# Optimization experiments

Hardware: AMD Instinct MI355X
Metric: run time of the kernel (lower is better)

The kernel has to match this reference:

```python
import jax, jax.numpy as jnp
import numpy as np

N = 100000       # nodes
E = 1600000      # edges
NFEAT = 128
NHID = 128
NCLASS = 64
NHEAD = 4
NLAYER = 3
LRELU_ALPHA = 0.2


def setup_inputs() -> dict:
    key = jax.random.key(0)
    ks = jax.random.split(key, 7)
    x = jax.random.normal(ks[0], (N, NFEAT), jnp.float32)
    edge_index = jax.random.randint(ks[1], (2, E), 0, N, jnp.int32)
    # xavier-uniform-ish init scales (gain for relu baked into scale roughly)
    Win = jax.random.normal(ks[2], (NFEAT, NHID), jnp.float32) * (2.0 / (NFEAT + NHID)) ** 0.5
    b_in = jnp.zeros((NHID,), jnp.float32)
    # per hidden layer, per head: a split into (src, dst) halves of the (1, 2*in) vector
    a_hid = jax.random.normal(ks[3], (NLAYER - 1, NHEAD, 2, NHID), jnp.float32) * 0.1
    W_hid = jax.random.normal(ks[4], (NLAYER - 1, NHEAD, NHID, NHID // NHEAD), jnp.float32) * (2.0 / (NHID + NHID // NHEAD)) ** 0.5
    a_out = jax.random.normal(ks[5], (2, NHID), jnp.float32) * 0.1
    W_out = jax.random.normal(ks[6], (NHID, NCLASS), jnp.float32) * (2.0 / (NHID + NCLASS)) ** 0.5
    return dict(x=x, edge_index=edge_index, Win=Win, b_in=b_in,
                a_hid=a_hid, W_hid=W_hid, a_out=a_out, W_out=W_out)


def _segment_softmax(logits, seg, n):
    # numerically stable softmax over groups defined by seg (axis 0)
    m = jax.ops.segment_max(logits, seg, num_segments=n)
    e = jnp.exp(logits - m[seg])
    s = jax.ops.segment_sum(e, seg, num_segments=n)
    return e / s[seg]


def _gat_conv(h, row, col, a, W):
    # h: [N, D]; a: [H, 2, D]; W: [H, D, Dh]
    n = h.shape[0]
    H = a.shape[0]
    s_src = h @ a[:, 0, :].T  # [N, H]
    s_dst = h @ a[:, 1, :].T  # [N, H]
    logits = jax.nn.leaky_relu(s_src[row] + s_dst[col], LRELU_ALPHA)  # [E, H]
    alpha = _segment_softmax(logits, row, n)  # softmax grouped by row (edge_index[0])
    h_col = h[col]  # [E, D] gathered once, reused per head
    outs = []
    for hd in range(H):  # small fixed head loop keeps peak memory at [E, D]
        agg = jax.ops.segment_sum(alpha[:, hd, None] * h_col, row, num_segments=n)  # [N, D]
        outs.append(agg @ W[hd])  # weight applied AFTER aggregation, as in source
    return jnp.concatenate(outs, axis=1)


def reference(x, edge_index, Win, b_in, a_hid, W_hid, a_out, W_out):
    row, col = edge_index[0], edge_index[1]
    h = jax.nn.elu(x @ Win + b_in)  # in_linear + ELU (dropout is identity in eval/p=0)
    for l in range(a_hid.shape[0]):
        h = jax.nn.elu(_gat_conv(h, row, col, a_hid[l], W_hid[l]))
    # final conv: single head to nclass, no activation
    return _gat_conv(h, row, col, a_out[None], W_out[None])
```

## Files before the change

kernel.cpp:

```cpp
#include <hip/hip_runtime.h>
#include <hip/hip_bf16.h>
#include <cstdint>
#include <cstddef>

#define LRELU_ALPHA 0.2f

typedef __attribute__((ext_vector_type(8))) short short8;
typedef __attribute__((ext_vector_type(4))) float f32x4;

__device__ __forceinline__ unsigned short f2bf(float f) {
    unsigned int u = __float_as_uint(f);
    unsigned int r = (u + 0x7fffu + ((u >> 16) & 1u)) >> 16;
    return (unsigned short)r;
}
__device__ __forceinline__ float bf2f(unsigned int lo16) {
    return __uint_as_float(lo16 << 16);
}
__device__ __forceinline__ unsigned int pk2(float a, float b) {
    return (unsigned int)f2bf(a) | ((unsigned int)f2bf(b) << 16);
}


__global__ void hist_k(const int* __restrict__ ei, int* __restrict__ counts,
                       int* __restrict__ rank, int E_) {
    int e = blockIdx.x * 256 + threadIdx.x;
    if (e < E_) {
        int r = ei[e];
        rank[e] = atomicAdd(&counts[r], 1);
    }
}

__global__ void scan_block_k(const int* __restrict__ counts, int* __restrict__ tmp,
                             int* __restrict__ bsum, int n) {
    __shared__ int s[256];
    int i = blockIdx.x * 256 + threadIdx.x;
    int v = (i < n) ? counts[i] : 0;
    s[threadIdx.x] = v;
    __syncthreads();
    for (int d = 1; d < 256; d <<= 1) {
        int t_ = (threadIdx.x >= d) ? s[threadIdx.x - d] : 0;
        __syncthreads();
        s[threadIdx.x] += t_;
        __syncthreads();
    }
    if (i < n) tmp[i] = s[threadIdx.x];
    if (threadIdx.x == 255) bsum[blockIdx.x] = s[255];
}

__global__ void scan_sums_k(int* bsum, int nb) {
    __shared__ int s[512];
    int v = ((int)threadIdx.x < nb) ? bsum[threadIdx.x] : 0;
    s[threadIdx.x] = v;
    __syncthreads();
    for (int d = 1; d < 512; d <<= 1) {
        int t_ = ((int)threadIdx.x >= d) ? s[threadIdx.x - d] : 0;
        __syncthreads();
        s[threadIdx.x] += t_;
        __syncthreads();
    }
    if ((int)threadIdx.x < nb) bsum[threadIdx.x] = s[threadIdx.x] - v;
}

__global__ void finalize_k(const int* __restrict__ tmp, const int* __restrict__ bsum,
                           int* __restrict__ off, int n) {
    int i = blockIdx.x * 256 + threadIdx.x;
    if (i < n) off[i + 1] = tmp[i] + bsum[blockIdx.x];
    if (i == 0) off[0] = 0;
}

__global__ void scatter_k(const int* __restrict__ ei, const int* __restrict__ rank,
                          const int* __restrict__ off, int* __restrict__ scol, int E_) {
    int e = blockIdx.x * 256 + threadIdx.x;
    if (e < E_) {
        int r = ei[e];
        int pos = off[r] + rank[e];
        scol[pos] = ei[E_ + e];
    }
}


template <int KJ, int HD>
__global__ void repack_wt(const float* __restrict__ src, unsigned short* __restrict__ wt) {
    int i = blockIdx.x * 256 + threadIdx.x;
    if (i < KJ * 128) {
        int n = i >> 7, k = i & 127;
        constexpr int JW = KJ / HD;
        int hd = n / JW, j = n % JW;
        wt[i] = f2bf(src[(hd * 128 + k) * JW + j]);
    }
}


template <int KJ, bool ELU_ACT, bool BIAS, bool BF16_OUT, bool ABF16>
__global__ __launch_bounds__(256) void gemm_mfma(const void* __restrict__ Xv,
                                                 const unsigned short* __restrict__ WT,
                                                 const float* __restrict__ bias,
                                                 void* __restrict__ Yv, int nRows) {
    constexpr int NT = KJ / 16;
    constexpr int WS = 136;
    __shared__ unsigned short sWT[KJ * WS];
    int t = threadIdx.x;
    for (int i = t; i < KJ * 16; i += 256) {
        int n = i >> 4, k8 = i & 15;
        uint4 v = *(const uint4*)&WT[n * 128 + k8 * 8];
        *(uint4*)&sWT[n * WS + k8 * 8] = v;
    }
    __syncthreads();

    int lane = t & 63;
    int wv = t >> 6;
    int m0 = blockIdx.x * 128 + wv * 32;
    int l16 = lane & 15;
    int q4 = lane >> 4;

    short8 afr[4][2];
    #pragma unroll
    for (int rt = 0; rt < 2; rt++) {
        int row = m0 + rt * 16 + l16;
        bool vr = row < nRows;
        if (ABF16) {
            const unsigned int* xp = (const unsigned int*)Xv + (size_t)row * 64 + q4 * 4;
            #pragma unroll
            for (int kk = 0; kk < 4; kk++) {
                uint4 u = make_uint4(0u, 0u, 0u, 0u);
                if (vr) u = *(const uint4*)(xp + kk * 16);
                afr[kk][rt] = *(short8*)&u;
            }
        } else {
            const float* xp = (const float*)Xv + (size_t)row * 128 + q4 * 8;
            #pragma unroll
            for (int kk = 0; kk < 4; kk++) {
                float4 a0 = make_float4(0.f, 0.f, 0.f, 0.f), a1 = a0;
                if (vr) {
                    a0 = *(const float4*)(xp + kk * 32);
                    a1 = *(const float4*)(xp + kk * 32 + 4);
                }
                unsigned int u[4];
                u[0] = pk2(a0.x, a0.y); u[1] = pk2(a0.z, a0.w);
                u[2] = pk2(a1.x, a1.y); u[3] = pk2(a1.z, a1.w);
                afr[kk][rt] = *(short8*)u;
            }
        }
    }

    f32x4 acc[2][NT] = {};
    #pragma unroll
    for (int kk = 0; kk < 4; kk++) {
        #pragma unroll
        for (int ct = 0; ct < NT; ct++) {
            int n = ct * 16 + l16;
            short8 bf = *(const short8*)&sWT[n * WS + kk * 32 + q4 * 8];
            #pragma unroll
            for (int rt = 0; rt < 2; rt++)
                acc[rt][ct] = __builtin_amdgcn_mfma_f32_16x16x32_bf16(afr[kk][rt], bf, acc[rt][ct], 0, 0, 0);
        }
    }

    #pragma unroll
    for (int rt = 0; rt < 2; rt++) {
        #pragma unroll
        for (int q = 0; q < 4; q++) {
            int row = m0 + rt * 16 + q4 * 4 + q;
            if (row >= nRows) continue;
            #pragma unroll
            for (int ct = 0; ct < NT; ct++) {
                int colc = ct * 16 + l16;
                float v = acc[rt][ct][q];
                if (BIAS) v += bias[colc];
                if (ELU_ACT) v = v > 0.f ? v : (__expf(v) - 1.f);
                if (BF16_OUT) ((unsigned short*)Yv)[(size_t)row * KJ + colc] = f2bf(v);
                else          ((float*)Yv)[(size_t)row * KJ + colc] = v;
            }
        }
    }
}


template <int H>
__global__ __launch_bounds__(256) void attn_scores_bf(const unsigned int* __restrict__ h2,
                                                      const float* __restrict__ a,
                                                      float* __restrict__ s_src,
                                                      float* __restrict__ s_dst, int n) {
    __shared__ float sa[H * 2 * 128];
    for (int i = threadIdx.x; i < H * 2 * 128; i += 256) sa[i] = a[i];
    __syncthreads();
    int lane = threadIdx.x & 63, wv = threadIdx.x >> 6;
    int node = blockIdx.x * 4 + wv;
    if (node >= n) return;
    unsigned int hv = h2[(size_t)node * 64 + lane];
    float v0 = bf2f(hv & 0xffffu), v1 = bf2f(hv >> 16);
    #pragma unroll
    for (int hd = 0; hd < H; hd++) {
        #pragma unroll
        for (int side = 0; side < 2; side++) {
            const float2 aa = *(const float2*)&sa[(hd * 2 + side) * 128 + 2 * lane];
            float p = v0 * aa.x + v1 * aa.y;
            #pragma unroll
            for (int s = 32; s > 0; s >>= 1) p += __shfl_xor(p, s);
            if (lane == 0) {
                float* dst = side ? s_dst : s_src;
                dst[node * H + hd] = p;
            }
        }
    }
}


template <int DHT, int H, bool ELU_ACT, int HN, bool BF16O>
__global__ __launch_bounds__(256) void edge_agg_v(const unsigned int* __restrict__ hW2,
                                                  const float* __restrict__ ssrc,
                                                  const float* __restrict__ sdst,
                                                  const int* __restrict__ off,
                                                  const int* __restrict__ scol,
                                                  void* __restrict__ outv,
                                                  const float* __restrict__ a_next,
                                                  float* __restrict__ ssrc_n,
                                                  float* __restrict__ sdst_n, int nRows) {
    constexpr int FPL = DHT / 16;
    constexpr int UPL = FPL / 2;
    constexpr int NC = (HN > 0) ? 2 * HN : 1;
    __shared__ float sAN[NC * 128];
    if (HN > 0) {
        for (int i = threadIdx.x; i < NC * 128; i += 256) sAN[i] = a_next[i];
        __syncthreads();
    }
    int lane = threadIdx.x & 63;
    int sub = lane & 15;
    int g = lane >> 4;
    int wv = threadIdx.x >> 6;
    int r = __builtin_amdgcn_readfirstlane(blockIdx.x * 4 + wv);
    if (r >= nRows) return;
    int begin = off[r], end = off[r + 1];

    int head = (H == 4) ? (sub >> 2) : 0;
    float ssl = ssrc[r * H + head];

    float acc[FPL] = {};
    float den = 0.f;

    for (int i = begin; i < end; i += 8) {
        int iA = i + g, iB = i + 4 + g;
        bool vA = iA < end, vB = iB < end;
        int cA = scol[vA ? iA : begin];
        int cB = scol[vB ? iB : begin];
        float sdA = sdst[cA * H + head];
        float sdB = sdst[cB * H + head];
        unsigned int hA[UPL], hB[UPL];
        int oA = cA * (DHT / 2) + sub * UPL;
        int oB = cB * (DHT / 2) + sub * UPL;
        if (UPL == 4) {
            *(uint4*)hA = *(const uint4*)&hW2[oA];
            *(uint4*)hB = *(const uint4*)&hW2[oB];
        } else {
            *(uint2*)hA = *(const uint2*)&hW2[oA];
            *(uint2*)hB = *(const uint2*)&hW2[oB];
        }
        float lgA = ssl + sdA; lgA = lgA > 0.f ? lgA : LRELU_ALPHA * lgA;
        float wA = vA ? __expf(lgA) : 0.f;
        float lgB = ssl + sdB; lgB = lgB > 0.f ? lgB : LRELU_ALPHA * lgB;
        float wB = vB ? __expf(lgB) : 0.f;
        den += wA + wB;
        #pragma unroll
        for (int q = 0; q < UPL; q++) {
            acc[2 * q]     = fmaf(wA, bf2f(hA[q] & 0xffffu), acc[2 * q]);
            acc[2 * q + 1] = fmaf(wA, bf2f(hA[q] >> 16),     acc[2 * q + 1]);
            acc[2 * q]     = fmaf(wB, bf2f(hB[q] & 0xffffu), acc[2 * q]);
            acc[2 * q + 1] = fmaf(wB, bf2f(hB[q] >> 16),     acc[2 * q + 1]);
        }
    }

    #pragma unroll
    for (int s = 16; s < 64; s <<= 1) {
        den += __shfl_xor(den, s);
        #pragma unroll
        for (int p = 0; p < FPL; p++) acc[p] += __shfl_xor(acc[p], s);
    }
    float inv = den > 0.f ? 1.f / den : 0.f;

    float v[FPL];
    #pragma unroll
    for (int p = 0; p < FPL; p++) {
        float tv = acc[p] * inv;
        if (ELU_ACT) tv = tv > 0.f ? tv : (__expf(tv) - 1.f);
        v[p] = tv;
    }

    if (DHT == 128) {
        if (BF16O)
            ((unsigned int*)outv)[(size_t)r * 64 + sub * 4 + g] = pk2(v[2 * g], v[2 * g + 1]);
        else
            *(float2*)&((float*)outv)[(size_t)r * 128 + sub * 8 + 2 * g] =
                make_float2(v[2 * g], v[2 * g + 1]);
    } else {
        ((float*)outv)[(size_t)r * DHT + sub * FPL + g] = v[g];
    }

    if (HN > 0) {
        constexpr int CPG = (HN == 4) ? 2 : 1;
        #pragma unroll
        for (int cc = 0; cc < CPG; cc++) {
            int c = (HN == 4) ? (g * 2 + cc) : (g & 1);
            const float* ap = &sAN[c * 128 + sub * FPL];
            float partial = 0.f;
            #pragma unroll
            for (int p = 0; p < FPL; p++) partial += v[p] * ap[p];
            #pragma unroll
            for (int s = 1; s < 16; s <<= 1) partial += __shfl_xor(partial, s);
            if (sub == 0 && (HN == 4 || g < 2)) {
                int hd = c >> 1;
                float* dst = (c & 1) ? sdst_n : ssrc_n;
                dst[r * HN + hd] = partial;
            }
        }
    }
}


extern "C" void kernel_launch(void* const* d_in, const int* in_sizes, int n_in,
                              void* d_out, int out_size, void* d_ws, size_t ws_size,
                              hipStream_t stream) {
    const float* x    = (const float*)d_in[0];
    const int*   ei   = (const int*)d_in[1];
    const float* Win  = (const float*)d_in[2];
    const float* bin  = (const float*)d_in[3];
    const float* ahid = (const float*)d_in[4];
    const float* Whid = (const float*)d_in[5];
    const float* aout = (const float*)d_in[6];
    const float* Wout = (const float*)d_in[7];
    float* out = (float*)d_out;

    const int N_ = in_sizes[0] / 128;
    const int E_ = in_sizes[1] / 2;

    char* p = (char*)d_ws;
    auto alloc = [&](size_t bytes) {
        char* q = p;
        p += (bytes + 511) & ~(size_t)511;
        return q;
    };
    int* counts = (int*)alloc((size_t)N_ * 4);
    int* tmp    = (int*)alloc((size_t)N_ * 4);
    int* rank   = (int*)alloc((size_t)E_ * 4);
    int* off    = (int*)alloc((size_t)(N_ + 1) * 4);
    int* bsum   = (int*)alloc(4096);
    int* scol   = (int*)alloc((size_t)(E_ + 8) * 4);
    float* ssrcA = (float*)alloc((size_t)N_ * 4 * 4);
    float* sdstA = (float*)alloc((size_t)N_ * 4 * 4);
    float* ssrcB = (float*)alloc((size_t)N_ * 4 * 4);
    float* sdstB = (float*)alloc((size_t)N_ * 4 * 4);
    unsigned int* hb  = (unsigned int*)alloc((size_t)N_ * 64 * 4);
    unsigned int* hWb = (unsigned int*)alloc((size_t)N_ * 64 * 4);
    unsigned short* WTb = (unsigned short*)alloc(128 * 128 * 2);

    int NB = (N_ + 255) / 256;
    int EB = (E_ + 255) / 256;
    int RT = (N_ + 127) / 128;
    int NW = (N_ + 3) / 4;

    hipMemsetAsync(counts, 0, (size_t)N_ * 4, stream);
    hist_k<<<EB, 256, 0, stream>>>(ei, counts, rank, E_);
    scan_block_k<<<NB, 256, 0, stream>>>(counts, tmp, bsum, N_);
    scan_sums_k<<<1, 512, 0, stream>>>(bsum, NB);
    finalize_k<<<NB, 256, 0, stream>>>(tmp, bsum, off, N_);
    scatter_k<<<EB, 256, 0, stream>>>(ei, rank, off, scol, E_);

    repack_wt<128, 1><<<64, 256, 0, stream>>>(Win, WTb);
    gemm_mfma<128, true, true, true, false><<<RT, 256, 0, stream>>>(x, WTb, bin, hb, N_);

    attn_scores_bf<4><<<NW, 256, 0, stream>>>(hb, ahid, ssrcA, sdstA, N_);

    repack_wt<128, 4><<<64, 256, 0, stream>>>(Whid, WTb);
    gemm_mfma<128, false, false, true, true><<<RT, 256, 0, stream>>>(hb, WTb, nullptr, hWb, N_);
    edge_agg_v<128, 4, true, 4, true><<<NW, 256, 0, stream>>>(
        hWb, ssrcA, sdstA, off, scol, hb, ahid + 4 * 2 * 128, ssrcB, sdstB, N_);

    repack_wt<128, 4><<<64, 256, 0, stream>>>(Whid + (size_t)4 * 128 * 32, WTb);
    gemm_mfma<128, false, false, true, true><<<RT, 256, 0, stream>>>(hb, WTb, nullptr, hWb, N_);
    edge_agg_v<128, 4, true, 1, true><<<NW, 256, 0, stream>>>(
        hWb, ssrcB, sdstB, off, scol, hb, aout, ssrcA, sdstA, N_);

    repack_wt<64, 1><<<32, 256, 0, stream>>>(Wout, WTb);
    gemm_mfma<64, false, false, true, true><<<RT, 256, 0, stream>>>(hb, WTb, nullptr, hWb, N_);
    edge_agg_v<64, 1, false, 0, false><<<NW, 256, 0, stream>>>(
        hWb, ssrcA, sdstA, off, scol, out, nullptr, nullptr, nullptr, N_);
}
```

Baseline: 522.4 us.

## Pad CSR rows to multiples of 8, use fp16 dot2 aggregation and exp2 scores

```diff
diff --git a/kernel.cpp b/kernel.cpp
--- a/kernel.cpp
+++ b/kernel.cpp
@@ -4,9 +4,11 @@
 #include <cstddef>
 
 #define LRELU_ALPHA 0.2f
+#define LOG2E 1.44269504088896f
 
 typedef __attribute__((ext_vector_type(8))) short short8;
 typedef __attribute__((ext_vector_type(4))) float f32x4;
+typedef _Float16 h2v __attribute__((ext_vector_type(2)));
 
 __device__ __forceinline__ unsigned short f2bf(float f) {
     unsigned int u = __float_as_uint(f);
@@ -18,6 +20,46 @@
 }
 __device__ __forceinline__ unsigned int pk2(float a, float b) {
     return (unsigned int)f2bf(a) | ((unsigned int)f2bf(b) << 16);
+}
+__device__ __forceinline__ float fexp2(float x) {
+#if __has_builtin(__builtin_amdgcn_exp2f)
+    return __builtin_amdgcn_exp2f(x);
+#else
+    return __expf(x * 0.69314718056f);
+#endif
+}
+__device__ __forceinline__ h2v pkrtz(float a, float b) {
+#if __has_builtin(__builtin_amdgcn_cvt_pkrtz)
+    auto r = __builtin_amdgcn_cvt_pkrtz(a, b);
+    union { decltype(r) i; h2v o; } u;
+    u.i = r;
+    return u.o;
+#else
+    h2v r; r.x = (_Float16)a; r.y = (_Float16)b; return r;
+#endif
+}
+__device__ __forceinline__ unsigned int pack_lo(unsigned int a, unsigned int b) {
+#if __has_builtin(__builtin_amdgcn_perm)
+    return __builtin_amdgcn_perm(a, b, 0x01000504u);
+#else
+    return (a & 0xffffu) | (b << 16);
+#endif
+}
+__device__ __forceinline__ unsigned int pack_hi(unsigned int a, unsigned int b) {
+#if __has_builtin(__builtin_amdgcn_perm)
+    return __builtin_amdgcn_perm(a, b, 0x03020706u);
+#else
+    return (a >> 16) | (b & 0xffff0000u);
+#endif
+}
+union U32H2 { unsigned int u; h2v h; };
+__device__ __forceinline__ float dot2f(unsigned int a, h2v w, float acc) {
+    U32H2 c; c.u = a;
+#if __has_builtin(__builtin_amdgcn_fdot2)
+    return __builtin_amdgcn_fdot2(c.h, w, acc, false);
+#else
+    return acc + (float)c.h.x * (float)w.x + (float)c.h.y * (float)w.y;
+#endif
 }
 
 
@@ -30,11 +72,25 @@
     }
 }
 
+__global__ void fill_pad_k(int* __restrict__ scol, float* __restrict__ sdA,
+                           float* __restrict__ sdB, float* __restrict__ sdC,
+                           unsigned int* __restrict__ hW, int N_, int total) {
+    int i = blockIdx.x * 256 + threadIdx.x;
+    if (i < total) scol[i] = N_;
+    if (blockIdx.x == 0) {
+        int t = threadIdx.x;
+        if (t < 4) { sdA[N_ * 4 + t] = -1e30f; sdB[N_ * 4 + t] = -1e30f; }
+        if (t == 4) sdC[N_] = -1e30f;
+        if (t >= 32 && t < 64)  hW[(size_t)N_ * 32 + (t - 32)] = 0u;
+        if (t >= 64 && t < 128) hW[(size_t)N_ * 64 + (t - 64)] = 0u;
+    }
+}
+
 __global__ void scan_block_k(const int* __restrict__ counts, int* __restrict__ tmp,
                              int* __restrict__ bsum, int n) {
     __shared__ int s[256];
     int i = blockIdx.x * 256 + threadIdx.x;
-    int v = (i < n) ? counts[i] : 0;
+    int v = (i < n) ? ((counts[i] + 7) & ~7) : 0;
     s[threadIdx.x] = v;
     __syncthreads();
     for (int d = 1; d < 256; d <<= 1) {
@@ -79,19 +135,31 @@
 }
 
 
-template <int KJ, int HD>
-__global__ void repack_wt(const float* __restrict__ src, unsigned short* __restrict__ wt) {
+__global__ void repack_all(const float* __restrict__ Win, const float* __restrict__ Whid,
+                           const float* __restrict__ Wout,
+                           unsigned short* __restrict__ W0, unsigned short* __restrict__ W1,
+                           unsigned short* __restrict__ W2, unsigned short* __restrict__ W3) {
     int i = blockIdx.x * 256 + threadIdx.x;
-    if (i < KJ * 128) {
+    if (i < 16384) {
         int n = i >> 7, k = i & 127;
-        constexpr int JW = KJ / HD;
-        int hd = n / JW, j = n % JW;
-        wt[i] = f2bf(src[(hd * 128 + k) * JW + j]);
-    }
-}
-
-
-template <int KJ, bool ELU_ACT, bool BIAS, bool BF16_OUT, bool ABF16>
+        W0[i] = f2bf(Win[k * 128 + n]);
+    } else if (i < 49152) {
+        int j = i - 16384;
+        int l = j >> 14;
+        int jj = j & 16383;
+        int n = jj >> 7, k = jj & 127;
+        int hd = n >> 5, c = n & 31;
+        float v = Whid[(size_t)l * 16384 + (hd * 128 + k) * 32 + c];
+        (l ? W2 : W1)[jj] = f2bf(v);
+    } else if (i < 57344) {
+        int j = i - 49152;
+        int n = j >> 7, k = j & 127;
+        W3[j] = f2bf(Wout[k * 64 + n]);
+    }
+}
+
+
+template <int KJ, bool ELU_ACT, bool BIAS, int OUTM, bool ABF16>
 __global__ __launch_bounds__(256) void gemm_mfma(const void* __restrict__ Xv,
                                                  const unsigned short* __restrict__ WT,
                                                  const float* __restrict__ bias,
@@ -168,8 +236,15 @@
                 float v = acc[rt][ct][q];
                 if (BIAS) v += bias[colc];
                 if (ELU_ACT) v = v > 0.f ? v : (__expf(v) - 1.f);
-                if (BF16_OUT) ((unsigned short*)Yv)[(size_t)row * KJ + colc] = f2bf(v);
-                else          ((float*)Yv)[(size_t)row * KJ + colc] = v;
+                if (OUTM == 1) {
+                    ((unsigned short*)Yv)[(size_t)row * KJ + colc] = f2bf(v);
+                } else if (OUTM == 2) {
+                    union { _Float16 hf; unsigned short us; } cv;
+                    cv.hf = (_Float16)v;
+                    ((unsigned short*)Yv)[(size_t)row * KJ + colc] = cv.us;
+                } else {
+                    ((float*)Yv)[(size_t)row * KJ + colc] = v;
+                }
             }
         }
     }
@@ -177,30 +252,35 @@
 
 
 template <int H>
-__global__ __launch_bounds__(256) void attn_scores_bf(const unsigned int* __restrict__ h2,
-                                                      const float* __restrict__ a,
-                                                      float* __restrict__ s_src,
-                                                      float* __restrict__ s_dst, int n) {
+__global__ __launch_bounds__(256) void attn_scores16(const unsigned int* __restrict__ h2,
+                                                     const float* __restrict__ a,
+                                                     float* __restrict__ s_src,
+                                                     float* __restrict__ s_dst, int n) {
     __shared__ float sa[H * 2 * 128];
-    for (int i = threadIdx.x; i < H * 2 * 128; i += 256) sa[i] = a[i];
+    for (int i = threadIdx.x; i < H * 2 * 128; i += 256) sa[i] = a[i] * LOG2E;
     __syncthreads();
     int lane = threadIdx.x & 63, wv = threadIdx.x >> 6;
-    int node = blockIdx.x * 4 + wv;
-    if (node >= n) return;
-    unsigned int hv = h2[(size_t)node * 64 + lane];
-    float v0 = bf2f(hv & 0xffffu), v1 = bf2f(hv >> 16);
-    #pragma unroll
-    for (int hd = 0; hd < H; hd++) {
-        #pragma unroll
-        for (int side = 0; side < 2; side++) {
-            const float2 aa = *(const float2*)&sa[(hd * 2 + side) * 128 + 2 * lane];
-            float p = v0 * aa.x + v1 * aa.y;
-            #pragma unroll
-            for (int s = 32; s > 0; s >>= 1) p += __shfl_xor(p, s);
-            if (lane == 0) {
-                float* dst = side ? s_dst : s_src;
-                dst[node * H + hd] = p;
-            }
+    int sub = lane & 15, g = lane >> 4;
+    int node = (blockIdx.x * 4 + wv) * 4 + g;
+    bool valid = node < n;
+    int nd = valid ? node : 0;
+    uint4 hv = *(const uint4*)&h2[(size_t)nd * 64 + sub * 4];
+    float f[8];
+    f[0] = bf2f(hv.x & 0xffffu); f[1] = bf2f(hv.x >> 16);
+    f[2] = bf2f(hv.y & 0xffffu); f[3] = bf2f(hv.y >> 16);
+    f[4] = bf2f(hv.z & 0xffffu); f[5] = bf2f(hv.z >> 16);
+    f[6] = bf2f(hv.w & 0xffffu); f[7] = bf2f(hv.w >> 16);
+    #pragma unroll
+    for (int c = 0; c < 2 * H; c++) {
+        const float* ap = &sa[c * 128 + sub * 8];
+        float p = 0.f;
+        #pragma unroll
+        for (int q = 0; q < 8; q++) p += f[q] * ap[q];
+        #pragma unroll
+        for (int s = 1; s < 16; s <<= 1) p += __shfl_xor(p, s);
+        if (sub == 0 && valid) {
+            float* dst = (c & 1) ? s_dst : s_src;
+            dst[node * H + (c >> 1)] = p;
         }
     }
 }
@@ -221,7 +301,7 @@
     constexpr int NC = (HN > 0) ? 2 * HN : 1;
     __shared__ float sAN[NC * 128];
     if (HN > 0) {
-        for (int i = threadIdx.x; i < NC * 128; i += 256) sAN[i] = a_next[i];
+        for (int i = threadIdx.x; i < NC * 128; i += 256) sAN[i] = a_next[i] * LOG2E;
         __syncthreads();
     }
     int lane = threadIdx.x & 63;
@@ -239,10 +319,8 @@
     float den = 0.f;
 
     for (int i = begin; i < end; i += 8) {
-        int iA = i + g, iB = i + 4 + g;
-        bool vA = iA < end, vB = iB < end;
-        int cA = scol[vA ? iA : begin];
-        int cB = scol[vB ? iB : begin];
+        int2 cc = *(const int2*)&scol[i + 2 * g];
+        int cA = cc.x, cB = cc.y;
         float sdA = sdst[cA * H + head];
         float sdB = sdst[cB * H + head];
         unsigned int hA[UPL], hB[UPL];
@@ -255,17 +333,16 @@
             *(uint2*)hA = *(const uint2*)&hW2[oA];
             *(uint2*)hB = *(const uint2*)&hW2[oB];
         }
-        float lgA = ssl + sdA; lgA = lgA > 0.f ? lgA : LRELU_ALPHA * lgA;
-        float wA = vA ? __expf(lgA) : 0.f;
-        float lgB = ssl + sdB; lgB = lgB > 0.f ? lgB : LRELU_ALPHA * lgB;
-        float wB = vB ? __expf(lgB) : 0.f;
+        float lgA = ssl + sdA;
+        float wA = fexp2(fmaxf(lgA, LRELU_ALPHA * lgA));
+        float lgB = ssl + sdB;
+        float wB = fexp2(fmaxf(lgB, LRELU_ALPHA * lgB));
         den += wA + wB;
+        h2v w2 = pkrtz(wA, wB);
         #pragma unroll
         for (int q = 0; q < UPL; q++) {
-            acc[2 * q]     = fmaf(wA, bf2f(hA[q] & 0xffffu), acc[2 * q]);
-            acc[2 * q + 1] = fmaf(wA, bf2f(hA[q] >> 16),     acc[2 * q + 1]);
-            acc[2 * q]     = fmaf(wB, bf2f(hB[q] & 0xffffu), acc[2 * q]);
-            acc[2 * q + 1] = fmaf(wB, bf2f(hB[q] >> 16),     acc[2 * q + 1]);
+            acc[2 * q]     = dot2f(pack_lo(hA[q], hB[q]), w2, acc[2 * q]);
+            acc[2 * q + 1] = dot2f(pack_hi(hA[q], hB[q]), w2, acc[2 * q + 1]);
         }
     }
 
@@ -343,44 +420,49 @@
     int* rank   = (int*)alloc((size_t)E_ * 4);
     int* off    = (int*)alloc((size_t)(N_ + 1) * 4);
     int* bsum   = (int*)alloc(4096);
-    int* scol   = (int*)alloc((size_t)(E_ + 8) * 4);
-    float* ssrcA = (float*)alloc((size_t)N_ * 4 * 4);
-    float* sdstA = (float*)alloc((size_t)N_ * 4 * 4);
-    float* ssrcB = (float*)alloc((size_t)N_ * 4 * 4);
-    float* sdstB = (float*)alloc((size_t)N_ * 4 * 4);
+    int* scol   = (int*)alloc((size_t)(E_ + 8 * N_ + 64) * 4);
+    float* ssrcA = (float*)alloc((size_t)(N_ + 1) * 4 * 4);
+    float* sdstA = (float*)alloc((size_t)(N_ + 1) * 4 * 4);
+    float* ssrcB = (float*)alloc((size_t)(N_ + 1) * 4 * 4);
+    float* sdstB = (float*)alloc((size_t)(N_ + 1) * 4 * 4);
+    float* ssrcC = (float*)alloc((size_t)(N_ + 1) * 4);
+    float* sdstC = (float*)alloc((size_t)(N_ + 1) * 4);
     unsigned int* hb  = (unsigned int*)alloc((size_t)N_ * 64 * 4);
-    unsigned int* hWb = (unsigned int*)alloc((size_t)N_ * 64 * 4);
-    unsigned short* WTb = (unsigned short*)alloc(128 * 128 * 2);
+    unsigned int* hWb = (unsigned int*)alloc((size_t)(N_ + 1) * 64 * 4);
+    unsigned short* WT0 = (unsigned short*)alloc(128 * 128 * 2);
+    unsigned short* WT1 = (unsigned short*)alloc(128 * 128 * 2);
+    unsigned short* WT2 = (unsigned short*)alloc(128 * 128 * 2);
+    unsigned short* WT3 = (unsigned short*)alloc(64 * 128 * 2);
 
     int NB = (N_ + 255) / 256;
     int EB = (E_ + 255) / 256;
     int RT = (N_ + 127) / 128;
     int NW = (N_ + 3) / 4;
-
-    hipMemsetAsync(counts, 0, (size_t)N_ * 4, stream);
+    int PADTOT = E_ + 8 * N_;
+
+    (void)hipMemsetAsync(counts, 0, (size_t)N_ * 4, stream);
     hist_k<<<EB, 256, 0, stream>>>(ei, counts, rank, E_);
+    fill_pad_k<<<(PADTOT + 255) / 256, 256, 0, stream>>>(scol, sdstA, sdstB, sdstC, hWb, N_, PADTOT);
     scan_block_k<<<NB, 256, 0, stream>>>(counts, tmp, bsum, N_);
     scan_sums_k<<<1, 512, 0, stream>>>(bsum, NB);
     finalize_k<<<NB, 256, 0, stream>>>(tmp, bsum, off, N_);
     scatter_k<<<EB, 256, 0, stream>>>(ei, rank, off, scol, E_);
 
-    repack_wt<128, 1><<<64, 256, 0, stream>>>(Win, WTb);
-    gemm_mfma<128, true, true, true, false><<<RT, 256, 0, stream>>>(x, WTb, bin, hb, N_);
-
-    attn_scores_bf<4><<<NW, 256, 0, stream>>>(hb, ahid, ssrcA, sdstA, N_);
-
-    repack_wt<128, 4><<<64, 256, 0, stream>>>(Whid, WTb);
-    gemm_mfma<128, false, false, true, true><<<RT, 256, 0, stream>>>(hb, WTb, nullptr, hWb, N_);
+    repack_all<<<224, 256, 0, stream>>>(Win, Whid, Wout, WT0, WT1, WT2, WT3);
+
+    gemm_mfma<128, true, true, 1, false><<<RT, 256, 0, stream>>>(x, WT0, bin, hb, N_);
+
+    attn_scores16<4><<<(N_ + 15) / 16, 256, 0, stream>>>(hb, ahid, ssrcA, sdstA, N_);
+
+    gemm_mfma<128, false, false, 2, true><<<RT, 256, 0, stream>>>(hb, WT1, nullptr, hWb, N_);
     edge_agg_v<128, 4, true, 4, true><<<NW, 256, 0, stream>>>(
         hWb, ssrcA, sdstA, off, scol, hb, ahid + 4 * 2 * 128, ssrcB, sdstB, N_);
 
-    repack_wt<128, 4><<<64, 256, 0, stream>>>(Whid + (size_t)4 * 128 * 32, WTb);
-    gemm_mfma<128, false, false, true, true><<<RT, 256, 0, stream>>>(hb, WTb, nullptr, hWb, N_);
+    gemm_mfma<128, false, false, 2, true><<<RT, 256, 0, stream>>>(hb, WT2, nullptr, hWb, N_);
     edge_agg_v<128, 4, true, 1, true><<<NW, 256, 0, stream>>>(
-        hWb, ssrcB, sdstB, off, scol, hb, aout, ssrcA, sdstA, N_);
-
-    repack_wt<64, 1><<<32, 256, 0, stream>>>(Wout, WTb);
-    gemm_mfma<64, false, false, true, true><<<RT, 256, 0, stream>>>(hb, WTb, nullptr, hWb, N_);
+        hWb, ssrcB, sdstB, off, scol, hb, aout, ssrcC, sdstC, N_);
+
+    gemm_mfma<64, false, false, 2, true><<<RT, 256, 0, stream>>>(hb, WT3, nullptr, hWb, N_);
     edge_agg_v<64, 1, false, 0, false><<<NW, 256, 0, stream>>>(
-        hWb, ssrcA, sdstA, off, scol, out, nullptr, nullptr, nullptr, N_);
-}
+        hWb, ssrcC, sdstC, off, scol, out, nullptr, nullptr, nullptr, N_);
+}
```

Result: faster. 480.8 us (-8.0%).
